# Kernel optimization log

Hardware: AMD Instinct MI355X
Metric: run time of the kernel (lower is better)

Reference implementation:

```python
import jax, jax.numpy as jnp
import numpy as np

STRIDE = 16
PRE_K = 600
POST_K = 100
NMS_T = 0.7


def _gen_anchors(base=16.0, ratios=(0.5, 1.0, 2.0), scales=(8.0, 16.0, 32.0)):
    a = []
    for s in scales:
        for r in ratios:
            w = base * s * (r ** 0.5)
            h = base * s / (r ** 0.5)
            a.append([-w / 2, -h / 2, w / 2, h / 2])
    return jnp.asarray(a, jnp.float32)  # [9,4]


def _conv(x, w, b, pad):
    y = jax.lax.conv_general_dilated(x, w, (1, 1), [(pad, pad), (pad, pad)],
                                     dimension_numbers=("NCHW", "OIHW", "NCHW"))
    return y + b[None, :, None, None]


def _decode(deltas, anchors):
    w = anchors[:, 2] - anchors[:, 0]
    h = anchors[:, 3] - anchors[:, 1]
    cx = anchors[:, 0] + 0.5 * w
    cy = anchors[:, 1] + 0.5 * h
    dx, dy, dw, dh = deltas[:, 0], deltas[:, 1], deltas[:, 2], deltas[:, 3]
    pcx = cx + dx * w
    pcy = cy + dy * h
    pw = w * jnp.exp(dw)
    ph = h * jnp.exp(dh)
    return jnp.stack([pcx - 0.5 * pw, pcy - 0.5 * ph,
                      pcx + 0.5 * pw, pcy + 0.5 * ph], axis=-1)


def _nms_keep(boxes, thresh):
    # boxes already sorted by score descending; returns bool keep mask [N]
    x1, y1, x2, y2 = boxes[:, 0], boxes[:, 1], boxes[:, 2], boxes[:, 3]
    area = (x2 - x1) * (y2 - y1)
    xx1 = jnp.maximum(x1[:, None], x1[None, :])
    yy1 = jnp.maximum(y1[:, None], y1[None, :])
    xx2 = jnp.minimum(x2[:, None], x2[None, :])
    yy2 = jnp.minimum(y2[:, None], y2[None, :])
    inter = jnp.maximum(xx2 - xx1, 0.0) * jnp.maximum(yy2 - yy1, 0.0)
    iou = inter / (area[:, None] + area[None, :] - inter)
    n = boxes.shape[0]
    idx = jnp.arange(n)

    def body(i, keep):
        suppress = keep[i] & (iou[i] > thresh) & (idx > i)
        return keep & ~suppress

    return jax.lax.fori_loop(0, n, body, jnp.ones((n,), bool))


def setup_inputs() -> dict:
    key = jax.random.key(0)
    ks = jax.random.split(key, 7)
    C_in, C_mid, A = 256, 256, 9
    feats = jax.random.normal(ks[0], (4, C_in, 128, 128), jnp.float32)
    conv_w = jax.random.normal(ks[1], (C_mid, C_in, 3, 3), jnp.float32) * 0.02
    conv_b = jnp.zeros((C_mid,), jnp.float32)
    cls_w = jax.random.normal(ks[2], (A, C_mid, 1, 1), jnp.float32) * 0.05
    cls_b = jnp.zeros((A,), jnp.float32)
    bbox_w = jax.random.normal(ks[3], (A * 4, C_mid, 1, 1), jnp.float32) * 0.02
    bbox_b = jnp.zeros((A * 4,), jnp.float32)
    return {"features": feats, "conv_w": conv_w, "conv_b": conv_b,
            "cls_w": cls_w, "cls_b": cls_b, "bbox_w": bbox_w, "bbox_b": bbox_b,
            "image_h": 2048, "image_w": 2048}


def reference(features, conv_w, conv_b, cls_w, cls_b, bbox_w, bbox_b, image_h, image_w):
    B, _, H, W = features.shape
    A = cls_w.shape[0]
    t = jax.nn.relu(_conv(features, conv_w, conv_b, 1))
    logits = _conv(t, cls_w, cls_b, 0)        # [B,A,H,W]
    bbox_deltas = _conv(t, bbox_w, bbox_b, 0)  # [B,4A,H,W]

    anchors = _gen_anchors()
    sx = jnp.arange(W, dtype=jnp.float32) * STRIDE
    sy = jnp.arange(H, dtype=jnp.float32) * STRIDE
    gy, gx = jnp.meshgrid(sy, sx, indexing="ij")
    shifts = jnp.stack([gx, gy, gx, gy], axis=2).reshape(-1, 4)  # [HW,4]
    anchors_all = (anchors[None, :, :] + shifts[:, None, :]).reshape(-1, 4)  # [HW*A,4]

    scores = jnp.transpose(logits, (0, 2, 3, 1)).reshape(B, -1)          # [B,HWA]
    deltas = jnp.transpose(bbox_deltas, (0, 2, 3, 1)).reshape(B, -1, 4)  # [B,HWA,4]

    img_w = jnp.float32(image_w)
    img_h = jnp.float32(image_h)

    def per_image(s, d):
        p = _decode(d, anchors_all)
        p = jnp.stack([jnp.clip(p[:, 0], 0.0, img_w),
                       jnp.clip(p[:, 1], 0.0, img_h),
                       jnp.clip(p[:, 2], 0.0, img_w),
                       jnp.clip(p[:, 3], 0.0, img_h)], axis=-1)
        _, topi = jax.lax.top_k(s, PRE_K)
        p = p[topi]                                # [PRE_K,4] sorted by score
        keep = _nms_keep(p, NMS_T)
        order = jnp.argsort(jnp.where(keep, 0, 1), stable=True)  # kept first, score order
        sel = order[:POST_K]
        valid = keep[sel]
        return p[sel] * valid[:, None].astype(p.dtype)  # zero-pad suppressed slots

    return jax.vmap(per_image)(scores, deltas)  # [B,POST_K,4]
```

## Files before the change

### kernel.cpp

```cpp
#include <hip/hip_runtime.h>
#include <cstdint>
#include <cstddef>

#define BB 4
#define CIN 256
#define HH 128
#define WW 128
#define NANCH (HH*WW*9)
#define PRE_K 600
#define POST_K 100
#define NMS_T 0.7f
#define CAND_CAP 8192
#define CCNT_STRIDE 16

typedef _Float16 f16x8 __attribute__((ext_vector_type(8)));
typedef float    f32x4 __attribute__((ext_vector_type(4)));

#define WS_SCORES 0
#define WS_DELTAS (BB*NANCH)
#define WS_WHI    (WS_DELTAS + BB*NANCH*4)
#define WS_WLO    (WS_WHI + 9*256*128)
#define WS_HIST   (WS_WLO + 9*256*128)
#define WS_CCNT   (WS_HIST + 8192)
#define WS_CAND   (WS_CCNT + 64)
#define WS_BOX6   (WS_CAND + BB*CAND_CAP*2)
#define WS_MROW   (WS_BOX6 + BB*PRE_K*4)
#define WS_PHI    (WS_MROW + BB*PRE_K*10*2)
#define WS_PLANE_F 8388608
#define WS_PLO    (WS_PHI + WS_PLANE_F)
#define WS_ZERO   (WS_PLO + WS_PLANE_F)
#define WS_TOTAL_FULL (WS_ZERO + 16)
#define WS_TOTAL_MIN  WS_PHI

__device__ inline unsigned score_key(float f) {
    unsigned u = __float_as_uint(f);
    return (u & 0x80000000u) ? ~u : (u | 0x80000000u);
}

__device__ inline void decode_box(unsigned idx, const float* __restrict__ deltas,
                                  int b, float fw, float fh, float* o4)
{
    const int a   = (int)(idx % 9u);
    const int n4  = (int)(idx / 9u);
    const int hh_ = n4 >> 7;
    const int ww_ = n4 & 127;
    const int si_ = a / 3, ri = a % 3;
    const double sq = (ri == 0) ? 0.70710678118654752440 : ((ri == 1) ? 1.0 : 1.41421356237309504880);
    const double sc = (si_ == 0) ? 8.0 : ((si_ == 1) ? 16.0 : 32.0);
    const float half_w = (float)(16.0 * sc * sq * 0.5);
    const float half_h = (float)(16.0 * sc / sq * 0.5);
    const float shx = 16.f * (float)ww_;
    const float shy = 16.f * (float)hh_;
    const float x1a = shx - half_w, x2a = shx + half_w;
    const float y1a = shy - half_h, y2a = shy + half_h;
    const float aw = x2a - x1a, ah = y2a - y1a;
    const float acx = x1a + 0.5f*aw, acy = y1a + 0.5f*ah;
    const float* d = deltas + ((size_t)b*NANCH + idx) * 4;
    const float dx = d[0], dy = d[1], dw = d[2], dh = d[3];
    const float pcx = acx + dx*aw;
    const float pcy = acy + dy*ah;
    const float pw  = aw * expf(dw);
    const float ph  = ah * expf(dh);
    o4[0] = fminf(fmaxf(pcx - 0.5f*pw, 0.f), fw);
    o4[1] = fminf(fmaxf(pcy - 0.5f*ph, 0.f), fh);
    o4[2] = fminf(fmaxf(pcx + 0.5f*pw, 0.f), fw);
    o4[3] = fminf(fmaxf(pcy + 0.5f*ph, 0.f), fh);
}

__global__ __launch_bounds__(256)
void prep_all(const float* __restrict__ feat, const float* __restrict__ convw,
              _Float16* __restrict__ pHi, _Float16* __restrict__ pLo,
              _Float16* __restrict__ whi, _Float16* __restrict__ wlo,
              float* __restrict__ zeroPg, unsigned* __restrict__ ghist,
              int prepBlocks)
{
    const int blk = blockIdx.x;
    if (blk < prepBlocks) {
        const int id = blk * 256 + threadIdx.x;
        if (blk == 0 && threadIdx.x < 16) zeroPg[threadIdx.x] = 0.f;
        const int gx = id & 127;
        const int gy = (id >> 7) & 127;
        const int ck = (id >> 14) & 7;
        const int b  = id >> 17;
        const int g  = (((gx + 1) >> 1) & 1) | (((gy + 1) & 1) << 1);
        const float* fb = feat + ((size_t)(b*256 + ck*32) << 14) + (gy << 7) + gx;
        f16x8 gh[4], gl[4];
        #pragma unroll
        for (int icg = 0; icg < 4; ++icg)
            #pragma unroll
            for (int k = 0; k < 8; ++k) {
                const float v = fb[(size_t)(icg*8 + k) << 14] * 16.f;
                const _Float16 h = (_Float16)v;
                gh[icg][k] = h;
                gl[icg][k] = (_Float16)(v - (float)h);
            }
        char* Hc = (char*)pHi + (size_t)id * 64;
        char* Lc = (char*)pLo + (size_t)id * 64;
        #pragma unroll
        for (int icg = 0; icg < 4; ++icg) {
            const int p = icg ^ g;
            *(f16x8*)(Hc + p*16) = gh[icg];
            *(f16x8*)(Lc + p*16) = gl[icg];
        }
    } else if (blk < prepBlocks + 256) {
        const int g = (blk - prepBlocks) * 256 + threadIdx.x;
        if (g >= 65536) return;
        const int oc = g >> 8, ic = g & 255;
        const int chunk = ic >> 5, icl = ic & 31;
        #pragma unroll
        for (int t = 0; t < 9; ++t) {
            const float v = convw[(size_t)g*9 + t] * 64.f;
            const _Float16 h = (_Float16)v;
            const _Float16 lo = (_Float16)(v - (float)h);
            const size_t o = (size_t)((t*8 + chunk)*256 + oc)*32 + icl;
            whi[o] = h;
            wlo[o] = lo;
        }
    } else {
        const int id = (blk - prepBlocks - 256) * 256 + threadIdx.x;
        if (id < 8256) ghist[id] = 0u;
    }
}

__global__ __launch_bounds__(512, 2)
void conv_mfma(const float* __restrict__ feat, const float* __restrict__ convb,
               const _Float16* __restrict__ whi, const _Float16* __restrict__ wlo,
               const float* __restrict__ clsw, const float* __restrict__ bboxw,
               const float* __restrict__ clsb, const float* __restrict__ bboxb,
               const _Float16* __restrict__ pHi, const _Float16* __restrict__ pLo,
               const float* __restrict__ zeroPg, unsigned* __restrict__ ghist,
               float* __restrict__ scores, float* __restrict__ deltas)
{
    __shared__ __align__(16) unsigned char smem[87040];
    float* sBias = (float*)(smem + 86016);

    const int bid = blockIdx.x;
    const int b  = bid >> 6;
    const int ty = (bid >> 3) & 7;
    const int tx = bid & 7;
    const int h0 = ty*16, c0 = tx*16;
    const int tid = threadIdx.x;
    const int w   = tid >> 6;
    const int wm  = w >> 1;
    const int wph = w & 1;
    const int l  = tid & 63;
    const int q  = l >> 4;
    const int c  = l & 15;

    const float* featb = feat + (size_t)b*CIN*HH*WW;
    const int wOff = (wm*64 + c)*32 + q*8;

    if (tid < 256) sBias[tid] = convb[tid] * 1024.f;

    int sdesc[3];
    #pragma unroll
    for (int it = 0; it < 3; ++it) {
        const int e = it*512 + tid;
        if (e < 1344) {
            const int Yl = e / 72, rem = e - Yl*72;
            const int Xl = rem >> 2, p = rem & 3;
            const int gy = h0 - 1 + Yl, gx = c0 - 1 + Xl;
            sdesc[it] = (((unsigned)gy < 128u) && ((unsigned)gx < 128u))
                        ? ((((gy << 7) + gx) << 6) + (p << 4)) : -1;
        } else sdesc[it] = -2;
    }

    auto stage = [&](int ck, int buf) {
        unsigned char* hb = smem + buf*21504;
        unsigned char* lb = smem + 43008 + buf*21504;
        if (pHi) {
            const size_t pb = ((size_t)(b*8 + ck)) << 20;
            #pragma unroll
            for (int pl = 0; pl < 2; ++pl) {
                const char* Ps = (const char*)(pl ? pLo : pHi) + pb;
                unsigned char* Pd = pl ? lb : hb;
                #pragma unroll
                for (int it = 0; it < 3; ++it) {
                    if (sdesc[it] != -2) {
                        const char* src = (sdesc[it] >= 0) ? Ps + sdesc[it]
                                                           : (const char*)zeroPg;
                        __builtin_amdgcn_global_load_lds(
                            (const __attribute__((address_space(1))) void*)src,
                            (__attribute__((address_space(3))) void*)(Pd + it*8192 + tid*16),
                            16, 0, 0);
                    }
                }
            }
        } else {
            const int ic0s = ck*32;
            for (int e = tid; e < 1296; e += 512) {
                const int icg = e / 324, s = e - icg*324;
                const int Y = s / 18, X = s - Y*18;
                const int gy = h0 - 1 + Y, gx = c0 - 1 + X;
                const int g = ((X >> 1) & 1) | ((Y & 1) << 1);
                const bool inb = ((unsigned)gy < 128u) && ((unsigned)gx < 128u);
                f16x8 hv, lv;
                #pragma unroll
                for (int k = 0; k < 8; ++k) {
                    float v = 0.f;
                    if (inb) v = featb[((size_t)(ic0s + icg*8 + k)*HH + gy)*WW + gx];
                    v *= 16.f;
                    const _Float16 h = (_Float16)v;
                    hv[k] = h;
                    lv[k] = (_Float16)(v - (float)h);
                }
                const int base = s*64 + ((icg ^ g) << 4);
                *(f16x8*)(hb + base) = hv;
                *(f16x8*)(lb + base) = lv;
            }
        }
    };

    stage(0, 0);
    __syncthreads();

    f32x4 acc[4][8];
    #pragma unroll
    for (int mf = 0; mf < 4; ++mf) {
        const f32x4 bv = *(const f32x4*)(sBias + (wm*64 + mf*16 + 4*q));
        #pragma unroll
        for (int nf = 0; nf < 8; ++nf) acc[mf][nf] = bv;
    }

    for (int chunk = 0; chunk < 8; ++chunk) {
        const int cur = chunk & 1;
        if (chunk + 1 < 8) stage(chunk + 1, cur ^ 1);
        const unsigned char* hb = smem + cur*21504;
        const unsigned char* lb = smem + 43008 + cur*21504;

        #pragma unroll 3
        for (int t = 0; t < 9; ++t) {
            const int ky = t / 3, kx = t - ky*3;
            const _Float16* pWh = whi + (size_t)(t*8 + chunk)*8192 + wOff;
            const _Float16* pWl = wlo + (size_t)(t*8 + chunk)*8192 + wOff;
            f16x8 ah[4], al[4];
            #pragma unroll
            for (int mf = 0; mf < 4; ++mf) {
                ah[mf] = *(const f16x8*)(const void*)(pWh + mf*512);
                al[mf] = *(const f16x8*)(const void*)(pWl + mf*512);
            }
            #pragma unroll
            for (int nfh = 0; nfh < 2; ++nfh) {
                f16x8 bh[4], bl[4];
                #pragma unroll
                for (int j = 0; j < 4; ++j) {
                    const int nf = nfh*4 + j;
                    const int Y = wph*8 + (nf >> 1)*2 + (c >> 3) + ky;
                    const int X = (nf & 1)*8 + (c & 7) + kx;
                    const int g = ((X >> 1) & 1) | ((Y & 1) << 1);
                    const int addr = (Y*18 + X)*64 + ((q ^ g) << 4);
                    bh[j] = *(const f16x8*)(hb + addr);
                    bl[j] = *(const f16x8*)(lb + addr);
                }
                #pragma unroll
                for (int mf = 0; mf < 4; ++mf)
                    #pragma unroll
                    for (int j = 0; j < 4; ++j) {
                        acc[mf][nfh*4+j] = __builtin_amdgcn_mfma_f32_16x16x32_f16(ah[mf], bh[j], acc[mf][nfh*4+j], 0, 0, 0);
                        acc[mf][nfh*4+j] = __builtin_amdgcn_mfma_f32_16x16x32_f16(ah[mf], bl[j], acc[mf][nfh*4+j], 0, 0, 0);
                        acc[mf][nfh*4+j] = __builtin_amdgcn_mfma_f32_16x16x32_f16(al[mf], bh[j], acc[mf][nfh*4+j], 0, 0, 0);
                    }
            }
        }
        __syncthreads();
    }

    #pragma unroll
    for (int mf = 0; mf < 4; ++mf)
        #pragma unroll
        for (int nf = 0; nf < 8; ++nf)
            #pragma unroll
            for (int r = 0; r < 4; ++r)
                acc[mf][nf][r] = fmaxf(acc[mf][nf][r], 0.f) * 0.0009765625f;

    float*    sW15  = (float*)smem;
    float*    sPart = (float*)(smem + 15360);
    unsigned* sHist = (unsigned*)(smem + 76800);

    for (int e = tid; e < 2048; e += 512) sHist[e] = 0u;

    for (int g = 0; g < 3; ++g) {
        __syncthreads();
        for (int e = tid; e < 3840; e += 512) {
            const int chl = e >> 8, o = e & 255;
            const int ch = g*15 + chl;
            sW15[e] = (ch < 9) ? clsw[ch*256 + o] : bboxw[(ch - 9)*256 + o];
        }
        __syncthreads();
        for (int chl = 0; chl < 15; ++chl) {
            f32x4 wv[4];
            #pragma unroll
            for (int mf = 0; mf < 4; ++mf)
                wv[mf] = *(const f32x4*)(sW15 + chl*256 + wm*64 + mf*16 + 4*q);
            float p[8];
            #pragma unroll
            for (int nf = 0; nf < 8; ++nf) {
                float s = 0.f;
                #pragma unroll
                for (int mf = 0; mf < 4; ++mf)
                    #pragma unroll
                    for (int r = 0; r < 4; ++r)
                        s += wv[mf][r] * acc[mf][nf][r];
                s += __shfl_xor(s, 16, 64);
                s += __shfl_xor(s, 32, 64);
                p[nf] = s;
            }
            const float v0 = (q == 0) ? p[0] : (q == 1) ? p[1] : (q == 2) ? p[2] : p[3];
            const float v1 = (q == 0) ? p[4] : (q == 1) ? p[5] : (q == 2) ? p[6] : p[7];
            sPart[(w*15 + chl)*128 + q*16 + c]      = v0;
            sPart[(w*15 + chl)*128 + 64 + q*16 + c] = v1;
        }
        __syncthreads();
        for (int e = tid; e < 3840; e += 512) {
            const int chl = e >> 8, pxg = e & 255;
            const int ph = pxg >> 7, pxl = pxg & 127;
            float s = 0.f;
            #pragma unroll
            for (int wmq = 0; wmq < 4; ++wmq)
                s += sPart[((wmq*2 + ph)*15 + chl)*128 + pxl];
            const int ch = g*15 + chl;
            s += (ch < 9) ? clsb[ch] : bboxb[ch - 9];
            const int nf = pxl >> 4, cc2 = pxl & 15;
            const int Y = ph*8 + (nf >> 1)*2 + (cc2 >> 3);
            const int X = (nf & 1)*8 + (cc2 & 7);
            const int gy = h0 + Y, gx = c0 + X;
            const int n4 = gy*WW + gx;
            if (ch < 9) {
                scores[(size_t)b*NANCH + n4*9 + ch] = s;
                atomicAdd(&sHist[score_key(s) >> 21], 1u);
            } else {
                const int cc = ch - 9;
                deltas[((size_t)b*NANCH + n4*9 + (cc >> 2))*4 + (cc & 3)] = s;
            }
        }
    }
    for (int e = tid; e < 2048; e += 512) {
        const unsigned cv = sHist[e];
        if (cv) atomicAdd(&ghist[b*2048 + e], cv);
    }
}

__device__ inline void find_thresh(const unsigned* hist, int NB, unsigned target, unsigned* shv)
{
    const int tid = threadIdx.x;
    if (tid < 64) {
        const int gsz = NB >> 5;
        unsigned gsum = 0;
        if (tid < 32)
            for (int k = 0; k < gsz; ++k)
                gsum += hist[tid*gsz + ((k + tid) & (gsz-1))];
        unsigned suf = gsum;
        #pragma unroll
        for (int d = 1; d < 32; d <<= 1) {
            const unsigned t = __shfl_down(suf, d, 64);
            if (tid + d < 32) suf += t;
        }
        const unsigned long long m = __ballot(tid < 32 && suf >= target);
        const int G = 63 - __clzll(m);
        unsigned caboveG = 0;
        { const unsigned t = __shfl(suf, G+1, 64); if (G < 31) caboveG = t; }
        unsigned h = 0;
        if (tid < gsz) h = hist[G*gsz + tid];
        unsigned wsuf = h;
        #pragma unroll
        for (int d = 1; d < 64; d <<= 1) {
            const unsigned t = __shfl_down(wsuf, d, 64);
            if (tid + d < gsz) wsuf += t;
        }
        const unsigned long long m2 = __ballot(tid < gsz && (caboveG + wsuf) >= target);
        const int L = 63 - __clzll(m2);
        if (tid == L) { shv[0] = (unsigned)(G*gsz + L); shv[1] = caboveG + wsuf - h; }
    }
}

__global__ __launch_bounds__(256)
void filter_kernel(const float* __restrict__ scores, const unsigned* __restrict__ ghist,
                   unsigned* __restrict__ ccnt, unsigned long long* __restrict__ cand)
{
    __shared__ unsigned h[2048];
    __shared__ unsigned shv[8];
    __shared__ unsigned long long lbuf[2304];
    __shared__ unsigned lcnt, gbase;
    const int blk = blockIdx.x;
    const int b = blk >> 6, s = blk & 63;
    const int tid = threadIdx.x;
    const unsigned* hb = ghist + b*2048;
    if (tid == 0) lcnt = 0u;
    for (int e = tid; e < 2048; e += 256) h[e] = hb[e];
    __syncthreads();
    find_thresh(h, 2048, PRE_K, shv);
    __syncthreads();
    const unsigned T1 = shv[0];
    const unsigned C  = shv[1] + h[T1];
    const float* si = scores + (size_t)b*NANCH + s*2304;
    if (C <= (unsigned)CAND_CAP) {
        #pragma unroll
        for (int k = 0; k < 9; ++k) {
            const int i = tid + k*256;
            const unsigned u = score_key(si[i]);
            if ((u >> 21) >= T1) {
                const unsigned p = atomicAdd(&lcnt, 1u);
                lbuf[p] = ((unsigned long long)(~u) << 32) | (unsigned)(s*2304 + i);
            }
        }
        __syncthreads();
        if (tid == 0) gbase = atomicAdd(&ccnt[b*CCNT_STRIDE], lcnt);
        __syncthreads();
        const unsigned nL = lcnt, base = gbase;
        for (unsigned e = tid; e < nL; e += 256)
            cand[(size_t)b*CAND_CAP + base + e] = lbuf[e];
    } else if (s == 0 && tid == 0) {
        ccnt[b*CCNT_STRIDE] = 0x7FFFFFFFu;
    }
}

__global__ __launch_bounds__(256)
void rank_kernel(const unsigned* __restrict__ ccnt, const unsigned long long* __restrict__ cand,
                 const float* __restrict__ deltas,
                 const int* __restrict__ imh, const int* __restrict__ imw,
                 float* __restrict__ boxes6)
{
    __shared__ unsigned long long cnd[CAND_CAP];
    const int blk = blockIdx.x;
    const int b = blk >> 5, s = blk & 31;
    const int tid = threadIdx.x;
    const unsigned n = ccnt[b*CCNT_STRIDE];
    if (n > (unsigned)CAND_CAP) return;
    const int e0 = s*256;
    if ((unsigned)e0 >= n) return;
    for (int e = tid; e < (int)n; e += 256)
        cnd[e] = cand[(size_t)b*CAND_CAP + e];
    __syncthreads();
    const int e = e0 + tid;
    if (e >= (int)n) return;
    const unsigned long long cv = cnd[e];
    unsigned rank = 0;
    for (int e2 = 0; e2 < (int)n; ++e2)
        rank += (cnd[e2] < cv) ? 1u : 0u;
    if (rank < PRE_K) {
        float o4[4];
        decode_box((unsigned)cv, deltas, b, (float)imw[0], (float)imh[0], o4);
        float* o = boxes6 + ((size_t)b*PRE_K + rank)*4;
        o[0] = o4[0]; o[1] = o4[1]; o[2] = o4[2]; o[3] = o4[3];
    }
}

__global__ __launch_bounds__(256)
void nmsmask_kernel(const unsigned* __restrict__ ccnt, const float* __restrict__ boxes6,
                    unsigned long long* __restrict__ gmrow)
{
    __shared__ float bx[PRE_K][4];
    const int blk = blockIdx.x;
    const int b = blk / 10, rg = blk - b*10;
    const int tid = threadIdx.x;
    const unsigned n = ccnt[b*CCNT_STRIDE];
    if (n > (unsigned)CAND_CAP) return;
    for (int e = tid; e < PRE_K*4; e += 256)
        bx[e >> 2][e & 3] = boxes6[(size_t)b*PRE_K*4 + e];
    __syncthreads();
    for (int item = tid; item < 600; item += 256) {
        const int i  = rg*60 + item/10;
        const int wj = item - (item/10)*10;
        unsigned long long m = 0ull;
        const int jbase = wj * 64;
        if (jbase + 63 > i) {
            const float xi1 = bx[i][0], yi1 = bx[i][1], xi2 = bx[i][2], yi2 = bx[i][3];
            const float ai = (xi2 - xi1) * (yi2 - yi1);
            for (int bit = 0; bit < 64; ++bit) {
                const int j = jbase + bit;
                if (j < PRE_K && j > i) {
                    const float xx1 = fmaxf(xi1, bx[j][0]);
                    const float yy1 = fmaxf(yi1, bx[j][1]);
                    const float xx2 = fminf(xi2, bx[j][2]);
                    const float yy2 = fminf(yi2, bx[j][3]);
                    const float inter = fmaxf(xx2 - xx1, 0.f) * fmaxf(yy2 - yy1, 0.f);
                    const float aj = (bx[j][2] - bx[j][0]) * (bx[j][3] - bx[j][1]);
                    const float iou = inter / (ai + aj - inter);
                    if (iou > NMS_T) m |= (1ull << bit);
                }
            }
        }
        gmrow[((size_t)b*PRE_K + i)*10 + wj] = m;
    }
}

__device__ inline unsigned long long shfl_u64(unsigned long long v, int src) {
    const int lo = __shfl((int)(v & 0xffffffffull), src, 64);
    const int hi = __shfl((int)(v >> 32), src, 64);
    return ((unsigned long long)(unsigned)hi << 32) | (unsigned)lo;
}

__global__ __launch_bounds__(1024)
void post_kernel(const float* __restrict__ scores, const float* __restrict__ deltas,
                 const unsigned* __restrict__ ccnt,
                 const float* __restrict__ boxes6, const unsigned long long* __restrict__ gmrow,
                 const int* __restrict__ imh, const int* __restrict__ imw,
                 float* __restrict__ out)
{
    __shared__ unsigned hist[2048];
    __shared__ unsigned long long arr[1024];
    __shared__ unsigned tiebuf[1024];
    __shared__ unsigned shv[8];
    __shared__ float bx[PRE_K][4];
    __shared__ unsigned long long mrow[PRE_K][10];
    __shared__ unsigned long long keepw[10];
    __shared__ unsigned wpfx[11];
    __shared__ int sel[POST_K];
    const int b = blockIdx.x, tid = threadIdx.x;
    const float* si = scores + (size_t)b*NANCH;

    const unsigned n = ccnt[b*CCNT_STRIDE];
    const bool fast = (n <= (unsigned)CAND_CAP);

    if (fast) {
        for (int e = tid; e < PRE_K*4; e += 1024)
            bx[e >> 2][e & 3] = boxes6[(size_t)b*PRE_K*4 + e];
        for (int e = tid; e < PRE_K*10; e += 1024)
            mrow[e/10][e - (e/10)*10] = gmrow[(size_t)b*PRE_K*10 + e];
        __syncthreads();
    } else {
        for (int i = tid; i < 2048; i += 1024) hist[i] = 0;
        __syncthreads();
        for (int i = tid; i < NANCH; i += 1024)
            atomicAdd(&hist[score_key(si[i]) >> 21], 1u);
        __syncthreads();
        find_thresh(hist, 2048, PRE_K, shv);
        __syncthreads();
        const unsigned T1 = shv[0], gtA = shv[1];
        __syncthreads();

        for (int i = tid; i < 2048; i += 1024) hist[i] = 0;
        __syncthreads();
        for (int i = tid; i < NANCH; i += 1024) {
            const unsigned u = score_key(si[i]);
            if ((u >> 21) == T1) atomicAdd(&hist[(u >> 10) & 0x7FFu], 1u);
        }
        __syncthreads();
        find_thresh(hist, 2048, PRE_K - gtA, shv);
        __syncthreads();
        const unsigned T2 = shv[0], gtB = shv[1];
        const unsigned top22 = (T1 << 11) | T2;
        __syncthreads();

        for (int i = tid; i < 1024; i += 1024) hist[i] = 0;
        __syncthreads();
        for (int i = tid; i < NANCH; i += 1024) {
            const unsigned u = score_key(si[i]);
            if ((u >> 10) == top22) atomicAdd(&hist[u & 0x3FFu], 1u);
        }
        __syncthreads();
        find_thresh(hist, 1024, PRE_K - gtA - gtB, shv);
        if (tid == 0) { shv[4] = 0; shv[5] = 0; }
        __syncthreads();
        const unsigned u_thr = (top22 << 10) | shv[0];
        const unsigned n_greater = gtA + gtB + shv[1];
        __syncthreads();

        for (int i = tid; i < NANCH; i += 1024) {
            const unsigned u = score_key(si[i]);
            if (u > u_thr) {
                const unsigned p = atomicAdd(&shv[4], 1u);
                arr[p] = ((unsigned long long)(~u) << 32) | (unsigned)i;
            } else if (u == u_thr) {
                const unsigned p = atomicAdd(&shv[5], 1u);
                if (p < 1024u) tiebuf[p] = (unsigned)i;
            }
        }
        __syncthreads();
        const unsigned cnt_tie = (shv[5] > 1024u) ? 1024u : shv[5];
        if ((unsigned)tid >= cnt_tie) tiebuf[tid] = 0xFFFFFFFFu;

        for (unsigned k = 2; k <= 1024; k <<= 1)
            for (unsigned j = k >> 1; j > 0; j >>= 1) {
                __syncthreads();
                const unsigned i = (unsigned)tid, ixj = i ^ j;
                if (ixj > i) {
                    const unsigned a = tiebuf[i], cc = tiebuf[ixj];
                    if ((a > cc) == ((i & k) == 0)) { tiebuf[i] = cc; tiebuf[ixj] = a; }
                }
            }
        __syncthreads();
        const unsigned ties_needed = PRE_K - n_greater;
        if ((unsigned)tid < ties_needed)
            arr[n_greater + tid] = ((unsigned long long)(~u_thr) << 32) | tiebuf[tid];
        if (tid >= PRE_K) arr[tid] = ~0ull;

        for (unsigned k = 2; k <= 1024; k <<= 1)
            for (unsigned j = k >> 1; j > 0; j >>= 1) {
                __syncthreads();
                const unsigned i = (unsigned)tid, ixj = i ^ j;
                if (ixj > i) {
                    const unsigned long long a = arr[i], cc = arr[ixj];
                    if ((a > cc) == ((i & k) == 0)) { arr[i] = cc; arr[ixj] = a; }
                }
            }
        __syncthreads();

        if (tid < PRE_K) {
            float o4[4];
            decode_box((unsigned)arr[tid], deltas, b, (float)imw[0], (float)imh[0], o4);
            bx[tid][0] = o4[0]; bx[tid][1] = o4[1]; bx[tid][2] = o4[2]; bx[tid][3] = o4[3];
        }
        __syncthreads();

        for (int item = tid; item < PRE_K*10; item += 1024) {
            const int i  = item / 10;
            const int wj = item - i*10;
            unsigned long long m = 0ull;
            const int jbase = wj * 64;
            if (jbase + 63 > i) {
                const float xi1 = bx[i][0], yi1 = bx[i][1], xi2 = bx[i][2], yi2 = bx[i][3];
                const float ai = (xi2 - xi1) * (yi2 - yi1);
                for (int bit = 0; bit < 64; ++bit) {
                    const int j = jbase + bit;
                    if (j < PRE_K && j > i) {
                        const float xx1 = fmaxf(xi1, bx[j][0]);
                        const float yy1 = fmaxf(yi1, bx[j][1]);
                        const float xx2 = fminf(xi2, bx[j][2]);
                        const float yy2 = fminf(yi2, bx[j][3]);
                        const float inter = fmaxf(xx2 - xx1, 0.f) * fmaxf(yy2 - yy1, 0.f);
                        const float aj = (bx[j][2] - bx[j][0]) * (bx[j][3] - bx[j][1]);
                        const float iou = inter / (ai + aj - inter);
                        if (iou > NMS_T) m |= (1ull << bit);
                    }
                }
            }
            mrow[i][wj] = m;
        }
        __syncthreads();
    }

    if (tid < 64) {
        const int lane = tid;
        unsigned long long kwv;
        if (lane < 9)       kwv = ~0ull;
        else if (lane == 9) kwv = (1ull << (PRE_K - 576)) - 1;
        else                kwv = 0ull;
        for (int w = 0; w < 10; ++w) {
            const int base = w*64;
            const int nb = (w == 9) ? (PRE_K - 576) : 64;
            if (lane == w) {
                for (int bit = 0; bit < nb; ++bit) {
                    const unsigned long long mm = mrow[base + bit][w];
                    if ((kwv >> bit) & 1ull) kwv &= ~mm;
                }
            }
            const unsigned long long fw = shfl_u64(kwv, w);
            if (lane > w && lane < 10) {
                for (int bit = 0; bit < nb; ++bit) {
                    const unsigned long long mm = mrow[base + bit][lane];
                    if ((fw >> bit) & 1ull) kwv &= ~mm;
                }
            }
        }
        if (lane < 10) keepw[lane] = kwv;
    }
    __syncthreads();
    if (tid == 0) {
        unsigned ccount = 0;
        #pragma unroll
        for (int w = 0; w < 10; ++w) { wpfx[w] = ccount; ccount += (unsigned)__popcll(keepw[w]); }
        wpfx[10] = ccount;
    }
    if (tid < POST_K) sel[tid] = -1;
    __syncthreads();
    if (tid < PRE_K) {
        const int w = tid >> 6, bit = tid & 63;
        const unsigned long long kw = keepw[w];
        if ((kw >> bit) & 1ull) {
            const unsigned rank = wpfx[w] + (unsigned)__popcll(kw & ((1ull << bit) - 1ull));
            if (rank < POST_K) sel[rank] = tid;
        }
    }
    __syncthreads();
    if (tid < POST_K) {
        const int s_ = sel[tid];
        float o0 = 0.f, o1 = 0.f, o2 = 0.f, o3 = 0.f;
        if (s_ >= 0) { o0 = bx[s_][0]; o1 = bx[s_][1]; o2 = bx[s_][2]; o3 = bx[s_][3]; }
        float* o = out + (size_t)b*POST_K*4 + tid*4;
        o[0] = o0; o[1] = o1; o[2] = o2; o[3] = o3;
    }
}

extern "C" void kernel_launch(void* const* d_in, const int* in_sizes, int n_in,
                              void* d_out, int out_size, void* d_ws, size_t ws_size,
                              hipStream_t stream) {
    const float* feat  = (const float*)d_in[0];
    const float* convw = (const float*)d_in[1];
    const float* convb = (const float*)d_in[2];
    const float* clsw  = (const float*)d_in[3];
    const float* clsb  = (const float*)d_in[4];
    const float* bboxw = (const float*)d_in[5];
    const float* bboxb = (const float*)d_in[6];
    const int*   imh   = (const int*)d_in[7];
    const int*   imw   = (const int*)d_in[8];

    if (ws_size < (size_t)WS_TOTAL_MIN * sizeof(float)) return;
    const bool use_prep = ws_size >= (size_t)WS_TOTAL_FULL * sizeof(float);

    float*    scores = (float*)d_ws + WS_SCORES;
    float*    deltas = (float*)d_ws + WS_DELTAS;
    _Float16* whi    = (_Float16*)((float*)d_ws + WS_WHI);
    _Float16* wlo    = (_Float16*)((float*)d_ws + WS_WLO);
    unsigned* ghist  = (unsigned*)((float*)d_ws + WS_HIST);
    unsigned* ccnt   = (unsigned*)((float*)d_ws + WS_CCNT);
    unsigned long long* cand = (unsigned long long*)((float*)d_ws + WS_CAND);
    float*    boxes6 = (float*)d_ws + WS_BOX6;
    unsigned long long* gmrow = (unsigned long long*)((float*)d_ws + WS_MROW);
    _Float16* pHi    = use_prep ? (_Float16*)((float*)d_ws + WS_PHI) : nullptr;
    _Float16* pLo    = use_prep ? (_Float16*)((float*)d_ws + WS_PLO) : nullptr;
    float*    zeroPg = use_prep ? ((float*)d_ws + WS_ZERO) : nullptr;
    float*    outp   = (float*)d_out;

    const int prepBlocks = use_prep ? 2048 : 0;
    prep_all<<<dim3(prepBlocks + 256 + 33), dim3(256), 0, stream>>>(
        feat, convw, pHi, pLo, whi, wlo, zeroPg, ghist, prepBlocks);
    conv_mfma<<<dim3(256), dim3(512), 0, stream>>>(feat, convb, whi, wlo, clsw, bboxw,
                                                   clsb, bboxb, pHi, pLo, zeroPg, ghist,
                                                   scores, deltas);
    filter_kernel<<<dim3(256), dim3(256), 0, stream>>>(scores, ghist, ccnt, cand);
    rank_kernel<<<dim3(128), dim3(256), 0, stream>>>(ccnt, cand, deltas, imh, imw, boxes6);
    nmsmask_kernel<<<dim3(40), dim3(256), 0, stream>>>(ccnt, boxes6, gmrow);
    post_kernel<<<dim3(BB), dim3(1024), 0, stream>>>(scores, deltas, ccnt, boxes6, gmrow,
                                                     imh, imw, outp);
}
```

Baseline: 359.2 us.

## Switch conv MFMA from 16x16x32 to 32x32x16 tiles with matching layouts

Replaces the 16x16x32 f16 MFMA tiling of the 3x3 conv with 32x32x16 MFMAs. The weight prep layout, the LDS swizzle pattern and the epilogue reduction are all reshaped to the new fragment mapping. Larger MFMA tiles cut the number of LDS fragment loads per flop and raise arithmetic intensity per instruction. The cost is a more complex swizzle and index mapping, and possible new LDS bank conflicts.

```diff
diff --git a/kernel.cpp b/kernel.cpp
--- a/kernel.cpp
+++ b/kernel.cpp
@@ -13,8 +13,9 @@
 #define CAND_CAP 8192
 #define CCNT_STRIDE 16
 
-typedef _Float16 f16x8 __attribute__((ext_vector_type(8)));
-typedef float    f32x4 __attribute__((ext_vector_type(4)));
+typedef _Float16 f16x8  __attribute__((ext_vector_type(8)));
+typedef float    f32x4  __attribute__((ext_vector_type(4)));
+typedef float    f32x16 __attribute__((ext_vector_type(16)));
 
 #define WS_SCORES 0
 #define WS_DELTAS (BB*NANCH)
@@ -82,7 +83,7 @@
         const int gy = (id >> 7) & 127;
         const int ck = (id >> 14) & 7;
         const int b  = id >> 17;
-        const int g  = (((gx + 1) >> 1) & 1) | (((gy + 1) & 1) << 1);
+        const int g  = (((gx + 1) >> 1) & 1) | ((((gx + 1) >> 2) & 1) << 1);
         const float* fb = feat + ((size_t)(b*256 + ck*32) << 14) + (gy << 7) + gx;
         f16x8 gh[4], gl[4];
         #pragma unroll
@@ -106,13 +107,15 @@
         const int g = (blk - prepBlocks) * 256 + threadIdx.x;
         if (g >= 65536) return;
         const int oc = g >> 8, ic = g & 255;
-        const int chunk = ic >> 5, icl = ic & 31;
+        const int ck = ic >> 5, icl = ic & 31;
+        const int kh = icl >> 4, kk = icl & 15;
+        const int kg = kk >> 3, j = kk & 7;
         #pragma unroll
         for (int t = 0; t < 9; ++t) {
             const float v = convw[(size_t)g*9 + t] * 64.f;
             const _Float16 h = (_Float16)v;
             const _Float16 lo = (_Float16)(v - (float)h);
-            const size_t o = (size_t)((t*8 + chunk)*256 + oc)*32 + icl;
+            const size_t o = (size_t)((((t*8 + ck)*2 + kh)*2 + kg)*256 + oc)*8 + j;
             whi[o] = h;
             wlo[o] = lo;
         }
@@ -144,11 +147,12 @@
     const int wm  = w >> 1;
     const int wph = w & 1;
     const int l  = tid & 63;
-    const int q  = l >> 4;
-    const int c  = l & 15;
+    const int kg = l >> 5;
+    const int yb = (l >> 4) & 1;
+    const int xb = l & 15;
+    const int ocl8 = (wm*64 + (l & 31)) * 8;
 
     const float* featb = feat + (size_t)b*CIN*HH*WW;
-    const int wOff = (wm*64 + c)*32 + q*8;
 
     if (tid < 256) sBias[tid] = convb[tid] * 1024.f;
 
@@ -192,7 +196,7 @@
                 const int icg = e / 324, s = e - icg*324;
                 const int Y = s / 18, X = s - Y*18;
                 const int gy = h0 - 1 + Y, gx = c0 - 1 + X;
-                const int g = ((X >> 1) & 1) | ((Y & 1) << 1);
+                const int g = ((X >> 1) & 1) | (((X >> 2) & 1) << 1);
                 const bool inb = ((unsigned)gy < 128u) && ((unsigned)gx < 128u);
                 f16x8 hv, lv;
                 #pragma unroll
@@ -214,12 +218,18 @@
     stage(0, 0);
     __syncthreads();
 
-    f32x4 acc[4][8];
+    f32x16 acc2[2][4];
     #pragma unroll
-    for (int mf = 0; mf < 4; ++mf) {
-        const f32x4 bv = *(const f32x4*)(sBias + (wm*64 + mf*16 + 4*q));
-        #pragma unroll
-        for (int nf = 0; nf < 8; ++nf) acc[mf][nf] = bv;
+    for (int of = 0; of < 2; ++of) {
+        #pragma unroll
+        for (int grp = 0; grp < 4; ++grp) {
+            const f32x4 bv = *(const f32x4*)(sBias + wm*64 + of*32 + grp*8 + 4*kg);
+            #pragma unroll
+            for (int pf = 0; pf < 4; ++pf)
+                #pragma unroll
+                for (int rr = 0; rr < 4; ++rr)
+                    acc2[of][pf][grp*4 + rr] = bv[rr];
+        }
     }
 
     for (int chunk = 0; chunk < 8; ++chunk) {
@@ -231,34 +241,33 @@
         #pragma unroll 3
         for (int t = 0; t < 9; ++t) {
             const int ky = t / 3, kx = t - ky*3;
-            const _Float16* pWh = whi + (size_t)(t*8 + chunk)*8192 + wOff;
-            const _Float16* pWl = wlo + (size_t)(t*8 + chunk)*8192 + wOff;
-            f16x8 ah[4], al[4];
+            const int X = xb + kx;
+            const int gsw = ((X >> 1) & 1) | (((X >> 2) & 1) << 1);
             #pragma unroll
-            for (int mf = 0; mf < 4; ++mf) {
-                ah[mf] = *(const f16x8*)(const void*)(pWh + mf*512);
-                al[mf] = *(const f16x8*)(const void*)(pWl + mf*512);
-            }
-            #pragma unroll
-            for (int nfh = 0; nfh < 2; ++nfh) {
+            for (int kh = 0; kh < 2; ++kh) {
+                const size_t so = (size_t)((((t*8 + chunk)*2 + kh)*2 + kg)*2048) + ocl8;
+                const _Float16* pWh = whi + so;
+                const _Float16* pWl = wlo + so;
+                f16x8 ah[2], al[2];
+                ah[0] = *(const f16x8*)(const void*)(pWh);
+                ah[1] = *(const f16x8*)(const void*)(pWh + 256);
+                al[0] = *(const f16x8*)(const void*)(pWl);
+                al[1] = *(const f16x8*)(const void*)(pWl + 256);
                 f16x8 bh[4], bl[4];
                 #pragma unroll
-                for (int j = 0; j < 4; ++j) {
-                    const int nf = nfh*4 + j;
-                    const int Y = wph*8 + (nf >> 1)*2 + (c >> 3) + ky;
-                    const int X = (nf & 1)*8 + (c & 7) + kx;
-                    const int g = ((X >> 1) & 1) | ((Y & 1) << 1);
-                    const int addr = (Y*18 + X)*64 + ((q ^ g) << 4);
-                    bh[j] = *(const f16x8*)(hb + addr);
-                    bl[j] = *(const f16x8*)(lb + addr);
+                for (int pf = 0; pf < 4; ++pf) {
+                    const int Y = wph*8 + pf*2 + yb + ky;
+                    const int addr = (Y*18 + X)*64 + (((kh*2 + kg) ^ gsw) << 4);
+                    bh[pf] = *(const f16x8*)(hb + addr);
+                    bl[pf] = *(const f16x8*)(lb + addr);
                 }
                 #pragma unroll
-                for (int mf = 0; mf < 4; ++mf)
+                for (int of = 0; of < 2; ++of)
                     #pragma unroll
-                    for (int j = 0; j < 4; ++j) {
-                        acc[mf][nfh*4+j] = __builtin_amdgcn_mfma_f32_16x16x32_f16(ah[mf], bh[j], acc[mf][nfh*4+j], 0, 0, 0);
-                        acc[mf][nfh*4+j] = __builtin_amdgcn_mfma_f32_16x16x32_f16(ah[mf], bl[j], acc[mf][nfh*4+j], 0, 0, 0);
-                        acc[mf][nfh*4+j] = __builtin_amdgcn_mfma_f32_16x16x32_f16(al[mf], bh[j], acc[mf][nfh*4+j], 0, 0, 0);
+                    for (int pf = 0; pf < 4; ++pf) {
+                        acc2[of][pf] = __builtin_amdgcn_mfma_f32_32x32x16_f16(ah[of], bh[pf], acc2[of][pf], 0, 0, 0);
+                        acc2[of][pf] = __builtin_amdgcn_mfma_f32_32x32x16_f16(ah[of], bl[pf], acc2[of][pf], 0, 0, 0);
+                        acc2[of][pf] = __builtin_amdgcn_mfma_f32_32x32x16_f16(al[of], bh[pf], acc2[of][pf], 0, 0, 0);
                     }
             }
         }
@@ -266,12 +275,12 @@
     }
 
     #pragma unroll
-    for (int mf = 0; mf < 4; ++mf)
-        #pragma unroll
-        for (int nf = 0; nf < 8; ++nf)
+    for (int of = 0; of < 2; ++of)
+        #pragma unroll
+        for (int pf = 0; pf < 4; ++pf)
             #pragma unroll
-            for (int r = 0; r < 4; ++r)
-                acc[mf][nf][r] = fmaxf(acc[mf][nf][r], 0.f) * 0.0009765625f;
+            for (int r = 0; r < 16; ++r)
+                acc2[of][pf][r] = fmaxf(acc2[of][pf][r], 0.f) * 0.0009765625f;
 
     float*    sW15  = (float*)smem;
     float*    sPart = (float*)(smem + 15360);
@@ -279,36 +288,40 @@
 
     for (int e = tid; e < 2048; e += 512) sHist[e] = 0u;
 
-    for (int g = 0; g < 3; ++g) {
+    for (int g2 = 0; g2 < 3; ++g2) {
         __syncthreads();
         for (int e = tid; e < 3840; e += 512) {
             const int chl = e >> 8, o = e & 255;
-            const int ch = g*15 + chl;
+            const int ch = g2*15 + chl;
             sW15[e] = (ch < 9) ? clsw[ch*256 + o] : bboxw[(ch - 9)*256 + o];
         }
         __syncthreads();
         for (int chl = 0; chl < 15; ++chl) {
-            f32x4 wv[4];
+            f32x4 wv[2][4];
             #pragma unroll
-            for (int mf = 0; mf < 4; ++mf)
-                wv[mf] = *(const f32x4*)(sW15 + chl*256 + wm*64 + mf*16 + 4*q);
-            float p[8];
+            for (int of = 0; of < 2; ++of)
+                #pragma unroll
+                for (int grp = 0; grp < 4; ++grp)
+                    wv[of][grp] = *(const f32x4*)(sW15 + chl*256 + wm*64 + of*32 + grp*8 + 4*kg);
+            float p[4];
             #pragma unroll
-            for (int nf = 0; nf < 8; ++nf) {
+            for (int pf = 0; pf < 4; ++pf) {
                 float s = 0.f;
                 #pragma unroll
-                for (int mf = 0; mf < 4; ++mf)
+                for (int of = 0; of < 2; ++of)
                     #pragma unroll
-                    for (int r = 0; r < 4; ++r)
-                        s += wv[mf][r] * acc[mf][nf][r];
-                s += __shfl_xor(s, 16, 64);
+                    for (int grp = 0; grp < 4; ++grp)
+                        #pragma unroll
+                        for (int rr = 0; rr < 4; ++rr)
+                            s += wv[of][grp][rr] * acc2[of][pf][grp*4 + rr];
                 s += __shfl_xor(s, 32, 64);
-                p[nf] = s;
-            }
-            const float v0 = (q == 0) ? p[0] : (q == 1) ? p[1] : (q == 2) ? p[2] : p[3];
-            const float v1 = (q == 0) ? p[4] : (q == 1) ? p[5] : (q == 2) ? p[6] : p[7];
-            sPart[(w*15 + chl)*128 + q*16 + c]      = v0;
-            sPart[(w*15 + chl)*128 + 64 + q*16 + c] = v1;
+                p[pf] = s;
+            }
+            if (kg == 0) {
+                #pragma unroll
+                for (int pf = 0; pf < 4; ++pf)
+                    sPart[(w*15 + chl)*128 + pf*32 + (l & 31)] = p[pf];
+            }
         }
         __syncthreads();
         for (int e = tid; e < 3840; e += 512) {
@@ -318,11 +331,10 @@
             #pragma unroll
             for (int wmq = 0; wmq < 4; ++wmq)
                 s += sPart[((wmq*2 + ph)*15 + chl)*128 + pxl];
-            const int ch = g*15 + chl;
+            const int ch = g2*15 + chl;
             s += (ch < 9) ? clsb[ch] : bboxb[ch - 9];
-            const int nf = pxl >> 4, cc2 = pxl & 15;
-            const int Y = ph*8 + (nf >> 1)*2 + (cc2 >> 3);
-            const int X = (nf & 1)*8 + (cc2 & 7);
+            const int Y = ph*8 + (pxl >> 5)*2 + ((pxl >> 4) & 1);
+            const int X = pxl & 15;
             const int gy = h0 + Y, gx = c0 + X;
             const int n4 = gy*WW + gx;
             if (ch < 9) {
```

Result: slower. 377.4 us (+5.1%).
